# Kernel optimization log

Hardware: AMD Instinct MI355X
Metric: run time of the kernel (lower is better)

## Reference

```python
import jax, jax.numpy as jnp
import numpy as np
import math

D_MODEL = 512
N_TOTAL = 1024
HW = 4096
EPSILON = 0.2
NUM_HEADS = 8
D_K = D_MODEL // NUM_HEADS
BATCH = 4


def setup_inputs() -> dict:
    rng = jax.random.key(0)
    ks = jax.random.split(rng, 16)
    s = 1.0 / math.sqrt(D_MODEL)
    inp = {
        "query": jax.random.normal(ks[0], (BATCH, N_TOTAL, D_MODEL), jnp.float32),
        "key": jax.random.normal(ks[1], (BATCH, HW, D_MODEL), jnp.float32),
        "value": jax.random.normal(ks[2], (BATCH, HW, D_MODEL), jnp.float32),
        "x_tilde": jax.random.uniform(ks[3], (HW, 2), jnp.float32),
        "x_hat": jax.random.uniform(ks[4], (N_TOTAL, HW, 2), jnp.float32),
        # torch nn.Linear params: W is (out, in), y = x @ W.T + b
        "Wq": jax.random.uniform(ks[5], (D_MODEL, D_MODEL), jnp.float32, -s, s),
        "bq": jax.random.uniform(ks[6], (D_MODEL,), jnp.float32, -s, s),
        "Wk": jax.random.uniform(ks[7], (D_MODEL, D_MODEL), jnp.float32, -s, s),
        "bk": jax.random.uniform(ks[8], (D_MODEL,), jnp.float32, -s, s),
        "Wv": jax.random.uniform(ks[9], (D_MODEL, D_MODEL), jnp.float32, -s, s),
        "bv": jax.random.uniform(ks[10], (D_MODEL,), jnp.float32, -s, s),
        "Wo": jax.random.uniform(ks[11], (D_MODEL, D_MODEL), jnp.float32, -s, s),
        "bo": jax.random.uniform(ks[12], (D_MODEL,), jnp.float32, -s, s),
    }
    return inp


def _geo_mask(x_tilde, x_hat):
    # x_tilde: (HW, 2), x_hat: (N_total, HW, 2)
    diff = x_tilde[None, :, :] - x_hat            # (N, HW, 2)
    dist = jnp.sqrt(jnp.sum(diff * diff, axis=-1))  # (N, HW)
    return jnp.where(dist < EPSILON, 0.0, -jnp.inf).astype(x_hat.dtype)


def reference(query, key, value, x_tilde, x_hat, Wq, bq, Wk, bk, Wv, bv, Wo, bo):
    B = query.shape[0]
    M_geo = _geo_mask(x_tilde, x_hat)  # (N, HW)

    def heads(x, W, b):
        y = x @ W.T + b                                   # (B, L, D)
        return y.reshape(B, -1, NUM_HEADS, D_K).transpose(0, 2, 1, 3)  # (B, H, L, dk)

    Q = heads(query, Wq, bq)   # (B, H, N, dk)
    K = heads(key, Wk, bk)     # (B, H, HW, dk)
    V = heads(value, Wv, bv)   # (B, H, HW, dk)

    scores = jnp.einsum("bhnd,bhmd->bhnm", Q, K) / math.sqrt(D_K)
    scores = scores + M_geo[None, None, :, :]
    attn = jax.nn.softmax(scores, axis=-1)                # (B, H, N, HW)
    ctx = jnp.einsum("bhnm,bhmd->bhnd", attn, V)          # (B, H, N, dk)
    ctx = ctx.transpose(0, 2, 1, 3).reshape(B, -1, D_MODEL)
    out = ctx @ Wo.T + bo                                 # (B, N, D)
    return out, attn
```

## Files before the change

### kernel.cpp

```cpp
#include <hip/hip_runtime.h>
#include <cstdint>
#include <cstddef>

typedef __attribute__((ext_vector_type(4))) float f32x4;
typedef __attribute__((ext_vector_type(8))) _Float16 h16x8;
typedef __attribute__((ext_vector_type(2))) _Float16 h16x2;
typedef __attribute__((ext_vector_type(8))) short s16x8;
typedef __attribute__((ext_vector_type(4))) short s16x4;
typedef unsigned short u16;
typedef unsigned long long u64;

static __device__ inline u16 f2h(float f) {
    _Float16 h = (_Float16)f;
    return __builtin_bit_cast(u16, h);
}

static __device__ inline f32x4 mfma16(h16x8 a, h16x8 b, f32x4 c) {
    return __builtin_amdgcn_mfma_f32_16x16x32_f16(a, b, c, 0, 0, 0);
}

static __device__ inline float redsum16(float v) {
    v += __shfl_xor(v, 1);
    v += __shfl_xor(v, 2);
    v += __shfl_xor(v, 4);
    v += __shfl_xor(v, 8);
    return v;
}

__global__ __launch_bounds__(256) void cvt_h_kernel(const float* __restrict__ src,
                                                    u16* __restrict__ dst, float scale) {
    int i = (blockIdx.x * 256 + threadIdx.x) * 4;
    f32x4 v = *(const f32x4*)(src + i);
    s16x4 o;
    o[0] = (short)f2h(v[0] * scale); o[1] = (short)f2h(v[1] * scale);
    o[2] = (short)f2h(v[2] * scale); o[3] = (short)f2h(v[3] * scale);
    *(s16x4*)(dst + i) = o;
}

__global__ __launch_bounds__(256) void mask_kernel(const float* __restrict__ xt,
                                                   const float* __restrict__ xh,
                                                   u64* __restrict__ mb) {
    int tid  = threadIdx.x;
    int lane = tid & 63;
    int wv   = blockIdx.x * 4 + (tid >> 6);
    int n    = wv >> 6;
    int mbk  = wv & 63;
    int m    = (mbk << 6) + lane;
    size_t hidx = ((size_t)n * 4096 + m) * 2;
    float dx = xt[2 * m]     - xh[hidx];
    float dy = xt[2 * m + 1] - xh[hidx + 1];
    bool p = sqrtf(dx * dx + dy * dy) < 0.2f;
    u64 bal = __ballot(p);
    if (lane == 0) mb[wv] = bal;
}

template <int INF32, int MODE, int LSHIFT>
__global__ __launch_bounds__(256) void proj_kernel(const void* __restrict__ Xv,
                                                   const u16* __restrict__ Wb,
                                                   const float* __restrict__ bias,
                                                   float bscale,
                                                   void* __restrict__ Yv) {
    __shared__ u16 aT[128 * 72];
    __shared__ u16 bT[128 * 72];

    int tid  = threadIdx.x;
    int lane = tid & 63, w = tid >> 6, q = lane >> 4, m15 = lane & 15;
    int wm = w >> 1, wn = w & 1;
    int m0 = blockIdx.x * 128, n0 = blockIdx.y * 128;
    int sRow = tid >> 1, sC = (tid & 1) * 32;

    f32x4 acc[4][4];
#pragma unroll
    for (int i = 0; i < 4; ++i)
#pragma unroll
        for (int j = 0; j < 4; ++j) { f32x4 z = {0.f, 0.f, 0.f, 0.f}; acc[i][j] = z; }

    for (int kb = 0; kb < 512; kb += 64) {
        if (INF32) {
            const float* X = (const float*)Xv;
#pragma unroll
            for (int j = 0; j < 8; ++j) {
                int col = sC + j * 4;
                f32x4 v = *(const f32x4*)(X + (size_t)(m0 + sRow) * 512 + kb + col);
                s16x4 o;
                o[0] = (short)f2h(v[0]); o[1] = (short)f2h(v[1]);
                o[2] = (short)f2h(v[2]); o[3] = (short)f2h(v[3]);
                *(s16x4*)(aT + sRow * 72 + col) = o;
            }
        } else {
            const u16* X = (const u16*)Xv;
#pragma unroll
            for (int j = 0; j < 4; ++j) {
                int col = sC + j * 8;
                s16x8 v = *(const s16x8*)(X + (size_t)(m0 + sRow) * 512 + kb + col);
                *(s16x8*)(aT + sRow * 72 + col) = v;
            }
        }
#pragma unroll
        for (int j = 0; j < 4; ++j) {
            int col = sC + j * 8;
            s16x8 v = *(const s16x8*)(Wb + (size_t)(n0 + sRow) * 512 + kb + col);
            *(s16x8*)(bT + sRow * 72 + col) = v;
        }
        __syncthreads();
#pragma unroll
        for (int kk = 0; kk < 2; ++kk) {
            h16x8 af[4], bf[4];
#pragma unroll
            for (int t = 0; t < 4; ++t) {
                af[t] = *(const h16x8*)(aT + (wm * 64 + t * 16 + m15) * 72 + kk * 32 + q * 8);
                bf[t] = *(const h16x8*)(bT + (wn * 64 + t * 16 + m15) * 72 + kk * 32 + q * 8);
            }
#pragma unroll
            for (int am = 0; am < 4; ++am)
#pragma unroll
                for (int bn = 0; bn < 4; ++bn)
                    acc[am][bn] = mfma16(af[am], bf[bn], acc[am][bn]);
        }
        __syncthreads();
    }

#pragma unroll
    for (int am = 0; am < 4; ++am) {
        int mg = m0 + wm * 64 + am * 16 + q * 4;
#pragma unroll
        for (int bn = 0; bn < 4; ++bn) {
            int col = n0 + wn * 64 + bn * 16 + m15;
            float bv = bias[col] * bscale;
            if (MODE == 2) {
                float* Y = (float*)Yv;
#pragma unroll
                for (int r = 0; r < 4; ++r)
                    Y[(size_t)(mg + r) * 512 + col] = acc[am][bn][r] + bv;
            } else if (MODE == 3) {
                u16* Y = (u16*)Yv;
                int hh = col >> 6, d = col & 63;
#pragma unroll
                for (int r = 0; r < 4; ++r) {
                    int m = mg + r;
                    int bb = m >> LSHIFT;
                    int nn = m & ((1 << LSHIFT) - 1);
                    Y[(((size_t)(bb * 8 + hh) << LSHIFT) + nn) * 64 + d] = f2h(acc[am][bn][r] + bv);
                }
            } else {
                u16* Yt = (u16*)Yv;
                int bidx = mg >> 12, hw0 = mg & 4095;
                int hh = col >> 6, d = col & 63;
                s16x4 o;
#pragma unroll
                for (int r = 0; r < 4; ++r) o[r] = (short)f2h(acc[am][bn][r] + bv);
                *(s16x4*)(Yt + ((size_t)((bidx << 3) + hh) * 64 + d) * 4096 + hw0) = o;
            }
        }
    }
}

__global__ __launch_bounds__(512, 2) void attn_kernel(const u16* __restrict__ Qh,
                                                      const u16* __restrict__ Kh,
                                                      const u16* __restrict__ Vt,
                                                      const u64* __restrict__ mbits,
                                                      float* __restrict__ attnO,
                                                      u16* __restrict__ ctxO) {
    __shared__ u64   smask[2048];
    __shared__ float sred[8][32];
    __shared__ float srowi[32];
    __shared__ u16   sps[8][2][16 * 72];
    __shared__ float sctx[2048];

    int tid  = threadIdx.x;
    int lane = tid & 63, w = tid >> 6, q = lane >> 4, m15 = lane & 15;
    int i = blockIdx.x;
    int jj = i >> 3;
    int bh = (i & 7) * 4 + (jj & 3);
    int n0 = (jj >> 2) * 32;
    int b = bh >> 3, h = bh & 7;

    for (int t = tid; t < 2048; t += 512) {
        smask[t] = mbits[(size_t)n0 * 64 + t];
        sctx[t]  = 0.f;
    }
    __syncthreads();

    h16x8 aQ[2][2];
#pragma unroll
    for (int g = 0; g < 2; ++g) {
        const u16* Qp = Qh + (((size_t)bh << 10) + n0 + g * 16 + m15) * 64 + q * 8;
        aQ[g][0] = *(const h16x8*)(Qp);
        aQ[g][1] = *(const h16x8*)(Qp + 32);
    }

    const u16* Kp = Kh + (((size_t)bh << 12) + (w << 9) + m15) * 64 + q * 8;
    const u16* Vp = Vt + (((size_t)bh << 6) + m15) * 4096 + (w << 9) + q * 8;
    const float L2E = 1.44269504f;

    unsigned st[8][4][2][2];
    float ls[2][4] = {{0.f,0.f,0.f,0.f},{0.f,0.f,0.f,0.f}};
    f32x4 ctxa[2][4];
#pragma unroll
    for (int g = 0; g < 2; ++g)
#pragma unroll
        for (int dt = 0; dt < 4; ++dt) { f32x4 z = {0.f, 0.f, 0.f, 0.f}; ctxa[g][dt] = z; }

#pragma unroll
    for (int cc = 0; cc < 8; ++cc) {
        int widx = w * 8 + cc;
        u64 mk[2][4];
#pragma unroll
        for (int g = 0; g < 2; ++g)
#pragma unroll
            for (int r = 0; r < 4; ++r) mk[g][r] = smask[(g * 16 + q * 4 + r) * 64 + widx];

#pragma unroll
        for (int tt = 0; tt < 4; ++tt) {
            const u16* kp = Kp + (size_t)(cc * 4 + tt) * (16 * 64);
            h16x8 b0 = *(const h16x8*)(kp);
            h16x8 b1 = *(const h16x8*)(kp + 32);
            f32x4 z = {0.f, 0.f, 0.f, 0.f};
            f32x4 c0 = mfma16(aQ[0][0], b0, mfma16(aQ[0][1], b1, z));
            f32x4 c1 = mfma16(aQ[1][0], b0, mfma16(aQ[1][1], b1, z));
            int bit = tt * 16 + m15;
            float p0[4], p1[4];
#pragma unroll
            for (int r = 0; r < 4; ++r) {
                p0[r] = ((mk[0][r] >> bit) & 1ull) ? exp2f(c0[r] * L2E) : 0.f;
                p1[r] = ((mk[1][r] >> bit) & 1ull) ? exp2f(c1[r] * L2E) : 0.f;
                ls[0][r] += p0[r];
                ls[1][r] += p1[r];
            }
            st[cc][tt][0][0] = __builtin_bit_cast(unsigned, __builtin_amdgcn_cvt_pkrtz(p0[0], p0[1]));
            st[cc][tt][0][1] = __builtin_bit_cast(unsigned, __builtin_amdgcn_cvt_pkrtz(p0[2], p0[3]));
            st[cc][tt][1][0] = __builtin_bit_cast(unsigned, __builtin_amdgcn_cvt_pkrtz(p1[0], p1[1]));
            st[cc][tt][1][1] = __builtin_bit_cast(unsigned, __builtin_amdgcn_cvt_pkrtz(p1[2], p1[3]));
#pragma unroll
            for (int g = 0; g < 2; ++g)
#pragma unroll
                for (int j = 0; j < 2; ++j) {
                    unsigned u = st[cc][tt][g][j];
                    sps[w][g][(q * 4 + 2 * j + 0) * 72 + tt * 16 + m15] = (u16)(u & 0xffffu);
                    sps[w][g][(q * 4 + 2 * j + 1) * 72 + tt * 16 + m15] = (u16)(u >> 16);
                }
        }
#pragma unroll
        for (int g = 0; g < 2; ++g)
#pragma unroll
            for (int half = 0; half < 2; ++half) {
                h16x8 aP = *(const h16x8*)(&sps[w][g][m15 * 72 + half * 32 + q * 8]);
#pragma unroll
                for (int dt = 0; dt < 4; ++dt) {
                    h16x8 bV = *(const h16x8*)(Vp + (size_t)dt * (16 * 4096) + cc * 64 + half * 32);
                    ctxa[g][dt] = mfma16(aP, bV, ctxa[g][dt]);
                }
            }
    }

#pragma unroll
    for (int g = 0; g < 2; ++g)
#pragma unroll
        for (int r = 0; r < 4; ++r) {
            float v = redsum16(ls[g][r]);
            if (m15 == 0) sred[w][g * 16 + q * 4 + r] = v;
        }
    __syncthreads();
    if (tid < 32) {
        float ss = 0.f;
#pragma unroll
        for (int ww = 0; ww < 8; ++ww) ss += sred[ww][tid];
        srowi[tid] = 1.0f / ss;
    }
    __syncthreads();
    float iv[2][4];
#pragma unroll
    for (int g = 0; g < 2; ++g)
#pragma unroll
        for (int r = 0; r < 4; ++r) iv[g][r] = srowi[g * 16 + q * 4 + r];

    float* aBp[2];
#pragma unroll
    for (int g = 0; g < 2; ++g)
        aBp[g] = attnO + (((size_t)bh << 10) + n0 + g * 16 + q * 4) * 4096 + (w << 9) + m15;

#pragma unroll
    for (int cc = 0; cc < 8; ++cc) {
#pragma unroll
        for (int tt = 0; tt < 4; ++tt) {
#pragma unroll
            for (int g = 0; g < 2; ++g)
#pragma unroll
                for (int j = 0; j < 2; ++j) {
                    h16x2 hv = __builtin_bit_cast(h16x2, st[cc][tt][g][j]);
                    float f0 = (float)hv[0] * iv[g][2 * j + 0];
                    float f1 = (float)hv[1] * iv[g][2 * j + 1];
                    __builtin_nontemporal_store(f0, aBp[g] + (size_t)(2 * j + 0) * 4096 + cc * 64 + tt * 16);
                    __builtin_nontemporal_store(f1, aBp[g] + (size_t)(2 * j + 1) * 4096 + cc * 64 + tt * 16);
                }
        }
    }

#pragma unroll
    for (int g = 0; g < 2; ++g)
#pragma unroll
        for (int dt = 0; dt < 4; ++dt)
#pragma unroll
            for (int r = 0; r < 4; ++r)
                atomicAdd(&sctx[(g * 16 + q * 4 + r) * 64 + dt * 16 + m15],
                          ctxa[g][dt][r] * iv[g][r]);
    __syncthreads();
    for (int t = tid; t < 2048; t += 512) {
        int rr = t >> 6, d = t & 63;
        ctxO[(((size_t)b << 10) + n0 + rr) * 512 + h * 64 + d] = f2h(sctx[t]);
    }
}

extern "C" void kernel_launch(void* const* d_in, const int* in_sizes, int n_in,
                              void* d_out, int out_size, void* d_ws, size_t ws_size,
                              hipStream_t stream) {
    (void)in_sizes; (void)n_in; (void)out_size; (void)ws_size;
    const float* query = (const float*)d_in[0];
    const float* key   = (const float*)d_in[1];
    const float* value = (const float*)d_in[2];
    const float* x_tilde = (const float*)d_in[3];
    const float* x_hat   = (const float*)d_in[4];
    const float* Wq = (const float*)d_in[5];  const float* bq = (const float*)d_in[6];
    const float* Wk = (const float*)d_in[7];  const float* bk = (const float*)d_in[8];
    const float* Wv = (const float*)d_in[9];  const float* bv = (const float*)d_in[10];
    const float* Wo = (const float*)d_in[11]; const float* bo = (const float*)d_in[12];

    char* ws = (char*)d_ws;
    u16* wq   = (u16*)(ws + 0);
    u16* wk   = (u16*)(ws + 524288);
    u16* wv   = (u16*)(ws + 1048576);
    u16* wo   = (u16*)(ws + 1572864);
    u16* Qh   = (u16*)(ws + 2097152);
    u16* Kh   = (u16*)(ws + 6291456);
    u16* Vtb  = (u16*)(ws + 23068672);
    u16* ctxb = (u16*)(ws + 39845888);
    u64* mbits = (u64*)(ws + 44040192);

    cvt_h_kernel<<<256, 256, 0, stream>>>(Wq, wq, 0.125f);
    cvt_h_kernel<<<256, 256, 0, stream>>>(Wk, wk, 1.0f);
    cvt_h_kernel<<<256, 256, 0, stream>>>(Wv, wv, 1.0f);
    cvt_h_kernel<<<256, 256, 0, stream>>>(Wo, wo, 1.0f);
    mask_kernel<<<16384, 256, 0, stream>>>(x_tilde, x_hat, mbits);

    proj_kernel<1, 3, 10><<<dim3(32, 4),  256, 0, stream>>>(query, wq, bq, 0.125f, Qh);
    proj_kernel<1, 3, 12><<<dim3(128, 4), 256, 0, stream>>>(key,   wk, bk, 1.0f,   Kh);
    proj_kernel<1, 1, 12><<<dim3(128, 4), 256, 0, stream>>>(value, wv, bv, 1.0f,   Vtb);

    float* attnO = (float*)d_out + 2097152;
    attn_kernel<<<1024, 512, 0, stream>>>(Qh, Kh, Vtb, mbits, attnO, ctxb);

    proj_kernel<0, 2, 10><<<dim3(32, 4), 256, 0, stream>>>(ctxb, wo, bo, 1.0f, d_out);
}
```

Baseline: 1.103 ms.

## Split attention into row-sum pass and recompute pass with vectorized stores

The kernel now runs a first pass over K that computes only the masked exp row sums. A second pass recomputes QK^T and the exponentials, writes the fp16 probabilities to LDS and runs the PV MFMAs. It then reads the probabilities back from LDS as 4-wide vectors and stores the normalized attention with 16-byte nontemporal stores. This removes the large per-thread register array of stored probabilities, whose pressure forced the occupancy-2 launch bound, and turns scattered scalar attention writes into coalesced vector writes. The cost is doubled QK^T MFMA and exp work, plus a dropped minimum-blocks hint.

```diff
diff --git a/kernel.cpp b/kernel.cpp
--- a/kernel.cpp
+++ b/kernel.cpp
@@ -4,7 +4,7 @@
 
 typedef __attribute__((ext_vector_type(4))) float f32x4;
 typedef __attribute__((ext_vector_type(8))) _Float16 h16x8;
-typedef __attribute__((ext_vector_type(2))) _Float16 h16x2;
+typedef __attribute__((ext_vector_type(4))) _Float16 h16x4;
 typedef __attribute__((ext_vector_type(8))) short s16x8;
 typedef __attribute__((ext_vector_type(4))) short s16x4;
 typedef unsigned short u16;
@@ -155,12 +155,12 @@
     }
 }
 
-__global__ __launch_bounds__(512, 2) void attn_kernel(const u16* __restrict__ Qh,
-                                                      const u16* __restrict__ Kh,
-                                                      const u16* __restrict__ Vt,
-                                                      const u64* __restrict__ mbits,
-                                                      float* __restrict__ attnO,
-                                                      u16* __restrict__ ctxO) {
+__global__ __launch_bounds__(512) void attn_kernel(const u16* __restrict__ Qh,
+                                                   const u16* __restrict__ Kh,
+                                                   const u16* __restrict__ Vt,
+                                                   const u64* __restrict__ mbits,
+                                                   float* __restrict__ attnO,
+                                                   u16* __restrict__ ctxO) {
     __shared__ u64   smask[2048];
     __shared__ float sred[8][32];
     __shared__ float srowi[32];
@@ -190,18 +190,68 @@
     }
 
     const u16* Kp = Kh + (((size_t)bh << 12) + (w << 9) + m15) * 64 + q * 8;
+    const float L2E = 1.44269504f;
+
+    float ls[2][4] = {{0.f,0.f,0.f,0.f},{0.f,0.f,0.f,0.f}};
+    for (int t4 = 0; t4 < 8; ++t4) {
+        int widx = w * 8 + t4;
+        u64 mk[2][4];
+#pragma unroll
+        for (int g = 0; g < 2; ++g)
+#pragma unroll
+            for (int r = 0; r < 4; ++r) mk[g][r] = smask[(g * 16 + q * 4 + r) * 64 + widx];
+#pragma unroll
+        for (int tt = 0; tt < 4; ++tt) {
+            const u16* kp = Kp + (size_t)(t4 * 4 + tt) * (16 * 64);
+            h16x8 b0 = *(const h16x8*)(kp);
+            h16x8 b1 = *(const h16x8*)(kp + 32);
+            f32x4 z = {0.f, 0.f, 0.f, 0.f};
+            f32x4 c0 = mfma16(aQ[0][0], b0, mfma16(aQ[0][1], b1, z));
+            f32x4 c1 = mfma16(aQ[1][0], b0, mfma16(aQ[1][1], b1, z));
+            int bit = tt * 16 + m15;
+#pragma unroll
+            for (int r = 0; r < 4; ++r) {
+                float p0 = ((mk[0][r] >> bit) & 1ull) ? exp2f(c0[r] * L2E) : 0.f;
+                float p1 = ((mk[1][r] >> bit) & 1ull) ? exp2f(c1[r] * L2E) : 0.f;
+                ls[0][r] += p0;
+                ls[1][r] += p1;
+            }
+        }
+    }
+#pragma unroll
+    for (int g = 0; g < 2; ++g)
+#pragma unroll
+        for (int r = 0; r < 4; ++r) {
+            float v = redsum16(ls[g][r]);
+            if (m15 == 0) sred[w][g * 16 + q * 4 + r] = v;
+        }
+    __syncthreads();
+    if (tid < 32) {
+        float ss = 0.f;
+#pragma unroll
+        for (int ww = 0; ww < 8; ++ww) ss += sred[ww][tid];
+        srowi[tid] = 1.0f / ss;
+    }
+    __syncthreads();
+    float iv[2][4];
+    float ivr[2][4];
+#pragma unroll
+    for (int g = 0; g < 2; ++g)
+#pragma unroll
+        for (int r = 0; r < 4; ++r) {
+            iv[g][r]  = srowi[g * 16 + q * 4 + r];
+            ivr[g][r] = srowi[g * 16 + r * 4 + q];
+        }
+
     const u16* Vp = Vt + (((size_t)bh << 6) + m15) * 4096 + (w << 9) + q * 8;
-    const float L2E = 1.44269504f;
-
-    unsigned st[8][4][2][2];
-    float ls[2][4] = {{0.f,0.f,0.f,0.f},{0.f,0.f,0.f,0.f}};
+    int c0l = m15 * 4;
+
     f32x4 ctxa[2][4];
 #pragma unroll
     for (int g = 0; g < 2; ++g)
 #pragma unroll
         for (int dt = 0; dt < 4; ++dt) { f32x4 z = {0.f, 0.f, 0.f, 0.f}; ctxa[g][dt] = z; }
 
-#pragma unroll
     for (int cc = 0; cc < 8; ++cc) {
         int widx = w * 8 + cc;
         u64 mk[2][4];
@@ -219,26 +269,13 @@
             f32x4 c0 = mfma16(aQ[0][0], b0, mfma16(aQ[0][1], b1, z));
             f32x4 c1 = mfma16(aQ[1][0], b0, mfma16(aQ[1][1], b1, z));
             int bit = tt * 16 + m15;
-            float p0[4], p1[4];
 #pragma unroll
             for (int r = 0; r < 4; ++r) {
-                p0[r] = ((mk[0][r] >> bit) & 1ull) ? exp2f(c0[r] * L2E) : 0.f;
-                p1[r] = ((mk[1][r] >> bit) & 1ull) ? exp2f(c1[r] * L2E) : 0.f;
-                ls[0][r] += p0[r];
-                ls[1][r] += p1[r];
-            }
-            st[cc][tt][0][0] = __builtin_bit_cast(unsigned, __builtin_amdgcn_cvt_pkrtz(p0[0], p0[1]));
-            st[cc][tt][0][1] = __builtin_bit_cast(unsigned, __builtin_amdgcn_cvt_pkrtz(p0[2], p0[3]));
-            st[cc][tt][1][0] = __builtin_bit_cast(unsigned, __builtin_amdgcn_cvt_pkrtz(p1[0], p1[1]));
-            st[cc][tt][1][1] = __builtin_bit_cast(unsigned, __builtin_amdgcn_cvt_pkrtz(p1[2], p1[3]));
-#pragma unroll
-            for (int g = 0; g < 2; ++g)
-#pragma unroll
-                for (int j = 0; j < 2; ++j) {
-                    unsigned u = st[cc][tt][g][j];
-                    sps[w][g][(q * 4 + 2 * j + 0) * 72 + tt * 16 + m15] = (u16)(u & 0xffffu);
-                    sps[w][g][(q * 4 + 2 * j + 1) * 72 + tt * 16 + m15] = (u16)(u >> 16);
-                }
+                float p0 = ((mk[0][r] >> bit) & 1ull) ? exp2f(c0[r] * L2E) : 0.f;
+                float p1 = ((mk[1][r] >> bit) & 1ull) ? exp2f(c1[r] * L2E) : 0.f;
+                sps[w][0][(q * 4 + r) * 72 + tt * 16 + m15] = f2h(p0);
+                sps[w][1][(q * 4 + r) * 72 + tt * 16 + m15] = f2h(p1);
+            }
         }
 #pragma unroll
         for (int g = 0; g < 2; ++g)
@@ -251,48 +288,20 @@
                     ctxa[g][dt] = mfma16(aP, bV, ctxa[g][dt]);
                 }
             }
-    }
-
-#pragma unroll
-    for (int g = 0; g < 2; ++g)
-#pragma unroll
-        for (int r = 0; r < 4; ++r) {
-            float v = redsum16(ls[g][r]);
-            if (m15 == 0) sred[w][g * 16 + q * 4 + r] = v;
-        }
-    __syncthreads();
-    if (tid < 32) {
-        float ss = 0.f;
-#pragma unroll
-        for (int ww = 0; ww < 8; ++ww) ss += sred[ww][tid];
-        srowi[tid] = 1.0f / ss;
-    }
-    __syncthreads();
-    float iv[2][4];
-#pragma unroll
-    for (int g = 0; g < 2; ++g)
-#pragma unroll
-        for (int r = 0; r < 4; ++r) iv[g][r] = srowi[g * 16 + q * 4 + r];
-
-    float* aBp[2];
-#pragma unroll
-    for (int g = 0; g < 2; ++g)
-        aBp[g] = attnO + (((size_t)bh << 10) + n0 + g * 16 + q * 4) * 4096 + (w << 9) + m15;
-
-#pragma unroll
-    for (int cc = 0; cc < 8; ++cc) {
-#pragma unroll
-        for (int tt = 0; tt < 4; ++tt) {
-#pragma unroll
-            for (int g = 0; g < 2; ++g)
-#pragma unroll
-                for (int j = 0; j < 2; ++j) {
-                    h16x2 hv = __builtin_bit_cast(h16x2, st[cc][tt][g][j]);
-                    float f0 = (float)hv[0] * iv[g][2 * j + 0];
-                    float f1 = (float)hv[1] * iv[g][2 * j + 1];
-                    __builtin_nontemporal_store(f0, aBp[g] + (size_t)(2 * j + 0) * 4096 + cc * 64 + tt * 16);
-                    __builtin_nontemporal_store(f1, aBp[g] + (size_t)(2 * j + 1) * 4096 + cc * 64 + tt * 16);
-                }
+#pragma unroll
+        for (int g = 0; g < 2; ++g) {
+            float* bp = attnO + (((size_t)bh << 10) + n0 + g * 16) * 4096 + (w << 9) + cc * 64 + c0l;
+#pragma unroll
+            for (int s = 0; s < 4; ++s) {
+                int row = s * 4 + q;
+                h16x4 hv = *(const h16x4*)(&sps[w][g][row * 72 + c0l]);
+                f32x4 o;
+                o[0] = (float)hv[0] * ivr[g][s];
+                o[1] = (float)hv[1] * ivr[g][s];
+                o[2] = (float)hv[2] * ivr[g][s];
+                o[3] = (float)hv[3] * ivr[g][s];
+                __builtin_nontemporal_store(o, (f32x4*)(bp + (size_t)row * 4096));
+            }
         }
     }
 
```

New measurement: 894.1 us. 1.23x faster.
